# Kernel tuning notes

Measured on AMD Instinct MI355X. Metric: run time of the kernel, lower is better.

Reference implementation:

```python
import jax, jax.numpy as jnp
import numpy as np

LATENT_DIM = 512


def setup_inputs() -> dict:
    key = jax.random.key(0)
    k1, k2, k3, k4 = jax.random.split(key, 4)
    B, C, H, W = 8, 256, 1, 65536  # W is a multiple of LATENT_DIM -> adaptive pool == binned mean
    x = jax.random.normal(k1, (B, C, H, W), dtype=jnp.float32)
    conv_w = jax.random.normal(k2, (1, C), dtype=jnp.float32) * (1.0 / np.sqrt(C))
    conv_b = jax.random.normal(k3, (1,), dtype=jnp.float32)
    eps = jax.random.normal(k4, (LATENT_DIM,), dtype=jnp.float32)  # reparam noise (vectorized rsample)
    return {"x": x, "conv_w": conv_w, "conv_b": conv_b, "eps": eps}


def reference(x, conv_w, conv_b, eps):
    B, C, H, W = x.shape
    L = eps.shape[0]
    # 1x1 Conv2d(channels -> 1): pure channel contraction
    o = jnp.einsum('bchw,oc->bohw', x, conv_w) + conv_b[None, :, None, None]  # [B,1,H,W]
    # AdaptiveAvgPool1d(L) over last dim; W % L == 0 so each bin averages W//L elems
    o_b = o.reshape(B, 1, H, L, W // L)
    mean = o_b.mean(axis=-1)               # [B,1,H,L]
    mean_sq = (o_b * o_b).mean(axis=-1)    # [B,1,H,L]
    std = jnp.sqrt(mean_sq - mean * mean)  # [B,1,H,L]
    # original loops over batch 0's concatenated [mean, std] vector and draws
    # z_i = Normal(mean_i, std_i).rsample(); vectorized reparameterization:
    m0 = mean[0, 0, 0]  # [L]
    s0 = std[0, 0, 0]   # [L]
    latent = m0 + s0 * eps
    return latent[None, :]  # [1, L]
```

## Files before the change

### kernel.cpp

```cpp
#include <hip/hip_runtime.h>
#include <hip/hip_bf16.h>

#define XW   65536
#define XC   256
#define XL   512
#define BIN  128

__global__ __launch_bounds__(1024) void statspool_kernel(
    const float* __restrict__ x,
    const float* __restrict__ cw,
    const float* __restrict__ cb,
    const float* __restrict__ eps,
    float* __restrict__ out)
{
    const int l  = blockIdx.x;
    const int t  = threadIdx.x;
    const int wi = t & 31;
    const int cg = t >> 5;

    const float4 wA = *(const float4*)(cw + (cg << 3));
    const float4 wB = *(const float4*)(cw + (cg << 3) + 4);
    const float wgt[8] = {wA.x, wA.y, wA.z, wA.w, wB.x, wB.y, wB.z, wB.w};

    const float* xp = x + (size_t)(cg << 3) * XW + l * BIN + (wi << 2);

    float4 acc = make_float4(0.f, 0.f, 0.f, 0.f);
    #pragma unroll
    for (int c = 0; c < 8; ++c) {
        const float4 v = *(const float4*)(xp + (size_t)c * XW);
        acc.x = fmaf(wgt[c], v.x, acc.x);
        acc.y = fmaf(wgt[c], v.y, acc.y);
        acc.z = fmaf(wgt[c], v.z, acc.z);
        acc.w = fmaf(wgt[c], v.w, acc.w);
    }

    __shared__ float part[32 * BIN];
    __shared__ float ob[BIN];
    *(float4*)(part + (cg << 7) + (wi << 2)) = acc;
    __syncthreads();

    if (t < BIN) {
        float s = 0.f;
        #pragma unroll
        for (int g = 0; g < 32; ++g) s += part[(g << 7) + t];
        ob[t] = s + cb[0];
    }
    __syncthreads();

    if (t < 64) {
        const float o0 = ob[t];
        const float o1 = ob[t + 64];
        float s  = o0 + o1;
        float sq = fmaf(o0, o0, o1 * o1);
        #pragma unroll
        for (int off = 32; off; off >>= 1) {
            s  += __shfl_down(s,  off);
            sq += __shfl_down(sq, off);
        }
        if (t == 0) {
            const float inv  = 1.0f / (float)BIN;
            const float mean = s * inv;
            const float msq  = sq * inv;
            const float var  = fmaxf(msq - mean * mean, 0.0f);
            out[l] = fmaf(sqrtf(var), eps[l], mean);
        }
    }
}

extern "C" void kernel_launch(void* const* d_in, const int* in_sizes, int n_in,
                              void* d_out, int out_size, void* d_ws, size_t ws_size,
                              hipStream_t stream) {
    const float* x   = (const float*)d_in[0];
    const float* cw  = (const float*)d_in[1];
    const float* cb  = (const float*)d_in[2];
    const float* eps = (const float*)d_in[3];
    float* out = (float*)d_out;

    statspool_kernel<<<dim3(XL), dim3(1024), 0, stream>>>(x, cw, cb, eps, out);
}
```

Measured before the change: 16.29 us.

## Process two bins per block with 1KB-wide contiguous row reads

Each block now covers two adjacent pooling bins (256 floats) instead of one, so a 64-lane wavefront reads a contiguous 1KB row segment per channel. Each thread loops over 16 channels strided by 16 instead of 8 consecutive ones. The grid is halved, which gives longer contiguous reads and fewer blocks to schedule. In exchange each thread issues more sequential loads, and there are fewer blocks to spread across CUs.

```diff
diff --git a/kernel.cpp b/kernel.cpp
--- a/kernel.cpp
+++ b/kernel.cpp
@@ -13,43 +13,42 @@
     const float* __restrict__ eps,
     float* __restrict__ out)
 {
-    const int l  = blockIdx.x;
+    const int bp = blockIdx.x;
     const int t  = threadIdx.x;
-    const int wi = t & 31;
-    const int cg = t >> 5;
+    const int wi = t & 63;
+    const int cg = t >> 6;
 
-    const float4 wA = *(const float4*)(cw + (cg << 3));
-    const float4 wB = *(const float4*)(cw + (cg << 3) + 4);
-    const float wgt[8] = {wA.x, wA.y, wA.z, wA.w, wB.x, wB.y, wB.z, wB.w};
-
-    const float* xp = x + (size_t)(cg << 3) * XW + l * BIN + (wi << 2);
+    const float* xp = x + (size_t)cg * XW + bp * 256 + (wi << 2);
 
     float4 acc = make_float4(0.f, 0.f, 0.f, 0.f);
     #pragma unroll
-    for (int c = 0; c < 8; ++c) {
-        const float4 v = *(const float4*)(xp + (size_t)c * XW);
-        acc.x = fmaf(wgt[c], v.x, acc.x);
-        acc.y = fmaf(wgt[c], v.y, acc.y);
-        acc.z = fmaf(wgt[c], v.z, acc.z);
-        acc.w = fmaf(wgt[c], v.w, acc.w);
+    for (int s = 0; s < 16; ++s) {
+        const float wc = cw[s * 16 + cg];
+        const float4 v = *(const float4*)(xp + (size_t)s * 16 * XW);
+        acc.x = fmaf(wc, v.x, acc.x);
+        acc.y = fmaf(wc, v.y, acc.y);
+        acc.z = fmaf(wc, v.z, acc.z);
+        acc.w = fmaf(wc, v.w, acc.w);
     }
 
-    __shared__ float part[32 * BIN];
-    __shared__ float ob[BIN];
-    *(float4*)(part + (cg << 7) + (wi << 2)) = acc;
+    __shared__ float part[16 * 256];
+    __shared__ float ob[256];
+    *(float4*)(part + (cg << 8) + (wi << 2)) = acc;
     __syncthreads();
 
-    if (t < BIN) {
+    if (t < 256) {
         float s = 0.f;
         #pragma unroll
-        for (int g = 0; g < 32; ++g) s += part[(g << 7) + t];
+        for (int g = 0; g < 16; ++g) s += part[(g << 8) + t];
         ob[t] = s + cb[0];
     }
     __syncthreads();
 
-    if (t < 64) {
-        const float o0 = ob[t];
-        const float o1 = ob[t + 64];
+    if (t < 128) {
+        const int bin = t >> 6;
+        const int ln  = t & 63;
+        const float o0 = ob[bin * BIN + ln];
+        const float o1 = ob[bin * BIN + ln + 64];
         float s  = o0 + o1;
         float sq = fmaf(o0, o0, o1 * o1);
         #pragma unroll
@@ -57,11 +56,12 @@
             s  += __shfl_down(s,  off);
             sq += __shfl_down(sq, off);
         }
-        if (t == 0) {
+        if (ln == 0) {
             const float inv  = 1.0f / (float)BIN;
             const float mean = s * inv;
             const float msq  = sq * inv;
             const float var  = fmaxf(msq - mean * mean, 0.0f);
+            const int l = bp * 2 + bin;
             out[l] = fmaf(sqrtf(var), eps[l], mean);
         }
     }
@@ -76,5 +76,5 @@
     const float* eps = (const float*)d_in[3];
     float* out = (float*)d_out;
 
-    statspool_kernel<<<dim3(XL), dim3(1024), 0, stream>>>(x, cw, cb, eps, out);
+    statspool_kernel<<<dim3(XL / 2), dim3(1024), 0, stream>>>(x, cw, cb, eps, out);
 }
```

New measurement: 18.15 us. 1.11x slower.
